# Kernel optimization log

Measured on AMD Instinct MI355X. Metric: run time of the kernel, lower is better.

Reference implementation:

```python
import jax, jax.numpy as jnp
import numpy as np

EPSILON = 1e-8
NUM_STEPS = 1000
S_OFFSET = 0.0001
POWER = 2
CLIPMAX = 0.999
B = 1048576


def _schedule():
    t = jnp.arange(0, NUM_STEPS + 1, dtype=jnp.float32)
    f_t = jnp.cos(np.pi / 2 * (t / NUM_STEPS + S_OFFSET) / (1 + S_OFFSET)) ** POWER
    alpha_bars = f_t / f_t[0]
    betas = jnp.concatenate([jnp.zeros([1], jnp.float32), 1.0 - alpha_bars[1:] / alpha_bars[:-1]])
    betas = jnp.minimum(betas, CLIPMAX)
    sigmas = jnp.sqrt(betas[1:] * ((1.0 - alpha_bars[:-1]) / (1.0 - alpha_bars[1:])))
    sigmas = jnp.concatenate([jnp.zeros([1], jnp.float32), sigmas])
    return alpha_bars, betas, sigmas


def setup_inputs() -> dict:
    key = jax.random.key(0)
    k1, k2, k3, k4, k5 = jax.random.split(key, 5)
    lt = jax.random.normal(k1, (B, 6), dtype=jnp.float32)
    predicted_l0 = jax.random.normal(k2, (B, 6), dtype=jnp.float32)
    pred_lattice = jax.random.normal(k3, (B, 3, 3), dtype=jnp.float32)
    z_noise = jax.random.normal(k4, (B, 6), dtype=jnp.float32)  # torch.randn_like(lt), frozen
    t = jax.random.randint(k5, (B,), 0, NUM_STEPS, dtype=jnp.int64)
    alpha_bars, betas, sigmas = _schedule()
    return {
        "lt": lt,
        "predicted_l0": predicted_l0,
        "pred_lattice": pred_lattice,
        "alpha_bars": alpha_bars,
        "betas": betas,
        "sigmas": sigmas,
        "z_noise": z_noise,
        "t": t,
    }


def reference(lt, predicted_l0, pred_lattice, alpha_bars, betas, sigmas, z_noise, t):
    # VP_lattice.reverse
    alpha = 1.0 - betas[t]
    alpha = jnp.maximum(alpha, 1.0 - betas[-2])  # clamp_min
    alpha_bar = alpha_bars[t]
    sigma = sigmas[t][:, None]

    # polar_decomposition: only the symmetric factor L_tilda = V diag(S) V^T is used
    _, S, Vt = jnp.linalg.svd(pred_lattice, full_matrices=False)  # (B,3),(B,3,3)
    L = jnp.einsum("bji,bj,bjk->bik", Vt, S, Vt)  # Vt^T @ diag(S) @ Vt
    L = (L + jnp.swapaxes(L, 1, 2)) / 2  # symmetrize

    # symmetric_matrix_to_vector: upper triangular incl. diagonal
    vec = jnp.stack([L[:, 0, 0], L[:, 0, 1], L[:, 0, 2], L[:, 1, 1], L[:, 1, 2], L[:, 2, 2]], axis=1)

    predicted_noise = lt - (vec + predicted_l0) / 2
    z = jnp.where((t > 1)[:, None], z_noise, jnp.zeros_like(z_noise))
    coef = (1.0 / jnp.sqrt(alpha + EPSILON))[:, None]
    scale = ((1.0 - alpha) / jnp.sqrt(1.0 - alpha_bar + EPSILON))[:, None]
    return coef * (lt - scale * predicted_noise) + sigma * z
```

## Files before the change

kernel.cpp:

```cpp
#include <hip/hip_runtime.h>


#define NUM_STEPS 1000
#define BLOCK 256

__global__ __launch_bounds__(BLOCK) void vp_lattice_kernel(
    const float* __restrict__ lt,
    const float* __restrict__ pl0,
    const float* __restrict__ plat,
    const float* __restrict__ alpha_bars,
    const float* __restrict__ betas,
    const float* __restrict__ sigmas,
    const float* __restrict__ z_noise,
    const int*   __restrict__ t,
    float* __restrict__ out,
    int n)
{
    __shared__ float sCoef[NUM_STEPS + 1];
    __shared__ float sScale[NUM_STEPS + 1];
    __shared__ float sSig[NUM_STEPS + 1];
    __shared__ __align__(16) float platT[BLOCK * 9];
    __shared__ __align__(16) float ltT[BLOCK * 6];
    __shared__ __align__(16) float p0T[BLOCK * 6];
    __shared__ __align__(16) float znT[BLOCK * 6];

    const int tid = threadIdx.x;
    const int rowBase = blockIdx.x * BLOCK;
    int rem = n - rowBase; if (rem > BLOCK) rem = BLOCK;

    if (rem == BLOCK) {
        const float4* g9 = reinterpret_cast<const float4*>(plat + (size_t)rowBase * 9);
        float4*       s9 = reinterpret_cast<float4*>(platT);
        for (int j = tid; j < BLOCK * 9 / 4; j += BLOCK) s9[j] = g9[j];

        const float4* gl = reinterpret_cast<const float4*>(lt + (size_t)rowBase * 6);
        float4*       sl = reinterpret_cast<float4*>(ltT);
        for (int j = tid; j < BLOCK * 6 / 4; j += BLOCK) sl[j] = gl[j];

        const float4* gp = reinterpret_cast<const float4*>(pl0 + (size_t)rowBase * 6);
        float4*       sp = reinterpret_cast<float4*>(p0T);
        for (int j = tid; j < BLOCK * 6 / 4; j += BLOCK) sp[j] = gp[j];

        const float4* gz = reinterpret_cast<const float4*>(z_noise + (size_t)rowBase * 6);
        float4*       sz = reinterpret_cast<float4*>(znT);
        for (int j = tid; j < BLOCK * 6 / 4; j += BLOCK) sz[j] = gz[j];
    } else {
        for (int j = tid; j < rem * 9; j += BLOCK) platT[j] = plat[(size_t)rowBase * 9 + j];
        for (int j = tid; j < rem * 6; j += BLOCK) {
            ltT[j] = lt[(size_t)rowBase * 6 + j];
            p0T[j] = pl0[(size_t)rowBase * 6 + j];
            znT[j] = z_noise[(size_t)rowBase * 6 + j];
        }
    }

    {
        float beta_last = betas[NUM_STEPS - 1];
        for (int j = tid; j <= NUM_STEPS; j += BLOCK) {
            float alpha = 1.0f - fminf(betas[j], beta_last);
            sCoef[j]  = 1.0f / sqrtf(alpha + 1e-8f);
            sScale[j] = (1.0f - alpha) / sqrtf(1.0f - alpha_bars[j] + 1e-8f);
            sSig[j]   = (j > 1) ? sigmas[j] : 0.0f;
        }
    }

    int ti = (tid < rem) ? t[rowBase + tid] : 0;

    __syncthreads();

    float ov0 = 0.f, ov1 = 0.f, ov2 = 0.f, ov3 = 0.f, ov4 = 0.f, ov5 = 0.f;

    if (tid < rem) {
        const float* pr = platT + tid * 9;
        float a00 = pr[0], a01 = pr[1], a02 = pr[2];
        float a10 = pr[3], a11 = pr[4], a12 = pr[5];
        float a20 = pr[6], a21 = pr[7], a22 = pr[8];

        float m00 = a00*a00 + a10*a10 + a20*a20;
        float m01 = a00*a01 + a10*a11 + a20*a21;
        float m02 = a00*a02 + a10*a12 + a20*a22;
        float m11 = a01*a01 + a11*a11 + a21*a21;
        float m12 = a01*a02 + a11*a12 + a21*a22;
        float m22 = a02*a02 + a12*a12 + a22*a22;

        float q  = (m00 + m11 + m22) * (1.0f/3.0f);
        float b00 = m00 - q, b11 = m11 - q, b22 = m22 - q;
        float p1 = m01*m01 + m02*m02 + m12*m12;
        float p2 = b00*b00 + b11*b11 + b22*b22 + 2.0f*p1;
        float p  = sqrtf(p2 * (1.0f/6.0f));
        float detB = b00*(b11*b22 - m12*m12)
                   - m01*(m01*b22 - m12*m02)
                   + m02*(m01*m12 - b11*m02);
        float pinv = 1.0f / fmaxf(p, 1e-20f);
        float r = 0.5f * detB * pinv * pinv * pinv;
        r = fminf(fmaxf(r, -1.0f), 1.0f);
        float phi = acosf(r) * (1.0f/3.0f);
        float mu1 = q + 2.0f*p*cosf(phi);
        float mu3 = q + 2.0f*p*cosf(phi + 2.0943951023931953f);
        float mu2 = 3.0f*q - mu1 - mu3;
        float l1 = sqrtf(fmaxf(mu1, 0.0f));
        float l2 = sqrtf(fmaxf(mu2, 0.0f));
        float l3 = sqrtf(fmaxf(mu3, 0.0f));

        float IU   = l1 + l2 + l3;
        float IIU  = l1*(l2 + l3) + l2*l3;
        float IIIU = l1*l2*l3;
        float denom = (l1 + l2) * (l1 + l3) * (l2 + l3);
        float dinv  = 1.0f / fmaxf(denom, 1e-25f);
        float sd = (IU*IU - IIU) * dinv;
        float td = IU * IIIU * dinv;
        float nd = -dinv;

        float mm00 = m00*m00 + m01*m01 + m02*m02;
        float mm01 = m00*m01 + m01*m11 + m02*m12;
        float mm02 = m00*m02 + m01*m12 + m02*m22;
        float mm11 = m01*m01 + m11*m11 + m12*m12;
        float mm12 = m01*m02 + m11*m12 + m12*m22;
        float mm22 = m02*m02 + m12*m12 + m22*m22;

        float v0 = nd*mm00 + sd*m00 + td;
        float v1 = nd*mm01 + sd*m01;
        float v2 = nd*mm02 + sd*m02;
        float v3 = nd*mm11 + sd*m11 + td;
        float v4 = nd*mm12 + sd*m12;
        float v5 = nd*mm22 + sd*m22 + td;

        float coef  = sCoef[ti];
        float scale = sScale[ti];
        float sig   = sSig[ti];

        const float2* l2v = reinterpret_cast<const float2*>(ltT) + tid * 3;
        const float2* p2v = reinterpret_cast<const float2*>(p0T) + tid * 3;
        const float2* z2v = reinterpret_cast<const float2*>(znT) + tid * 3;
        float lv[6], pv[6], zv[6];
        float2 w;
        w = l2v[0]; lv[0]=w.x; lv[1]=w.y;
        w = l2v[1]; lv[2]=w.x; lv[3]=w.y;
        w = l2v[2]; lv[4]=w.x; lv[5]=w.y;
        w = p2v[0]; pv[0]=w.x; pv[1]=w.y;
        w = p2v[1]; pv[2]=w.x; pv[3]=w.y;
        w = p2v[2]; pv[4]=w.x; pv[5]=w.y;
        w = z2v[0]; zv[0]=w.x; zv[1]=w.y;
        w = z2v[1]; zv[2]=w.x; zv[3]=w.y;
        w = z2v[2]; zv[4]=w.x; zv[5]=w.y;

        float vv[6] = {v0, v1, v2, v3, v4, v5};
        float ovv[6];
#pragma unroll
        for (int c = 0; c < 6; ++c) {
            float lc = lv[c];
            float pn = lc - 0.5f * (vv[c] + pv[c]);
            ovv[c] = coef * (lc - scale * pn) + sig * zv[c];
        }
        ov0 = ovv[0]; ov1 = ovv[1]; ov2 = ovv[2];
        ov3 = ovv[3]; ov4 = ovv[4]; ov5 = ovv[5];
    }

    __syncthreads();

    if (tid < rem) {
        float2* o2 = reinterpret_cast<float2*>(platT) + tid * 3;
        o2[0] = make_float2(ov0, ov1);
        o2[1] = make_float2(ov2, ov3);
        o2[2] = make_float2(ov4, ov5);
    }

    __syncthreads();

    if (rem == BLOCK) {
        const float4* so = reinterpret_cast<const float4*>(platT);
        float4*       go = reinterpret_cast<float4*>(out + (size_t)rowBase * 6);
        for (int j = tid; j < BLOCK * 6 / 4; j += BLOCK) go[j] = so[j];
    } else {
        for (int j = tid; j < rem * 6; j += BLOCK) out[(size_t)rowBase * 6 + j] = platT[j];
    }
}

extern "C" void kernel_launch(void* const* d_in, const int* in_sizes, int n_in,
                              void* d_out, int out_size, void* d_ws, size_t ws_size,
                              hipStream_t stream) {
    const float* lt         = (const float*)d_in[0];
    const float* pl0        = (const float*)d_in[1];
    const float* plat       = (const float*)d_in[2];
    const float* alpha_bars = (const float*)d_in[3];
    const float* betas      = (const float*)d_in[4];
    const float* sigmas     = (const float*)d_in[5];
    const float* z_noise    = (const float*)d_in[6];
    const int*   t          = (const int*)d_in[7];
    float* out = (float*)d_out;

    int n = in_sizes[0] / 6;
    int grid = (n + BLOCK - 1) / BLOCK;
    vp_lattice_kernel<<<grid, BLOCK, 0, stream>>>(
        lt, pl0, plat, alpha_bars, betas, sigmas, z_noise, t, out, n);
}
```

Before: 171.4 us.

## Precompute schedule table, drop LDS staging for 6-wide arrays, use fast acos/cos

A small pre-kernel folds the per-timestep coefficients into three tables (A, B, sigma) in workspace, which each block copies into LDS instead of recomputing sqrt/div per entry. The lt, predicted_l0, z_noise loads and the output store now go directly through per-thread float2 accesses rather than being staged through shared memory, which removes two barriers and shrinks LDS use. acosf is replaced by a polynomial approximation and cos/div by fast intrinsics, and launch bounds request higher occupancy. The trade-offs are less coalesced strided global accesses, an extra kernel launch, and reduced accuracy in the eigenvalue computation.

```diff
diff --git a/kernel.cpp b/kernel.cpp
--- a/kernel.cpp
+++ b/kernel.cpp
@@ -2,9 +2,31 @@
 
 
 #define NUM_STEPS 1000
+#define TBL 1008
 #define BLOCK 256
 
-__global__ __launch_bounds__(BLOCK) void vp_lattice_kernel(
+__global__ __launch_bounds__(256) void sched_kernel(
+    const float* __restrict__ alpha_bars,
+    const float* __restrict__ betas,
+    const float* __restrict__ sigmas,
+    float* __restrict__ ws)
+{
+    int j = blockIdx.x * blockDim.x + threadIdx.x;
+    if (j >= TBL) return;
+    if (j <= NUM_STEPS) {
+        float beta_last = betas[NUM_STEPS - 1];
+        float alpha = 1.0f - fminf(betas[j], beta_last);
+        float coef  = 1.0f / sqrtf(alpha + 1e-8f);
+        float scale = (1.0f - alpha) / sqrtf(1.0f - alpha_bars[j] + 1e-8f);
+        ws[j]           = coef * (1.0f - scale);
+        ws[TBL + j]     = 0.5f * coef * scale;
+        ws[2 * TBL + j] = (j > 1) ? sigmas[j] : 0.0f;
+    } else {
+        ws[j] = 0.0f; ws[TBL + j] = 0.0f; ws[2 * TBL + j] = 0.0f;
+    }
+}
+
+__global__ __launch_bounds__(BLOCK, 6) void vp_lattice_kernel(
     const float* __restrict__ lt,
     const float* __restrict__ pl0,
     const float* __restrict__ plat,
@@ -14,15 +36,14 @@
     const float* __restrict__ z_noise,
     const int*   __restrict__ t,
     float* __restrict__ out,
-    int n)
+    int n,
+    const float* __restrict__ ws,
+    int use_ws)
 {
-    __shared__ float sCoef[NUM_STEPS + 1];
-    __shared__ float sScale[NUM_STEPS + 1];
-    __shared__ float sSig[NUM_STEPS + 1];
+    __shared__ __align__(16) float sA[TBL];
+    __shared__ __align__(16) float sB[TBL];
+    __shared__ __align__(16) float sS[TBL];
     __shared__ __align__(16) float platT[BLOCK * 9];
-    __shared__ __align__(16) float ltT[BLOCK * 6];
-    __shared__ __align__(16) float p0T[BLOCK * 6];
-    __shared__ __align__(16) float znT[BLOCK * 6];
 
     const int tid = threadIdx.x;
     const int rowBase = blockIdx.x * BLOCK;
@@ -31,35 +52,39 @@
     if (rem == BLOCK) {
         const float4* g9 = reinterpret_cast<const float4*>(plat + (size_t)rowBase * 9);
         float4*       s9 = reinterpret_cast<float4*>(platT);
-        for (int j = tid; j < BLOCK * 9 / 4; j += BLOCK) s9[j] = g9[j];
-
-        const float4* gl = reinterpret_cast<const float4*>(lt + (size_t)rowBase * 6);
-        float4*       sl = reinterpret_cast<float4*>(ltT);
-        for (int j = tid; j < BLOCK * 6 / 4; j += BLOCK) sl[j] = gl[j];
-
-        const float4* gp = reinterpret_cast<const float4*>(pl0 + (size_t)rowBase * 6);
-        float4*       sp = reinterpret_cast<float4*>(p0T);
-        for (int j = tid; j < BLOCK * 6 / 4; j += BLOCK) sp[j] = gp[j];
-
-        const float4* gz = reinterpret_cast<const float4*>(z_noise + (size_t)rowBase * 6);
-        float4*       sz = reinterpret_cast<float4*>(znT);
-        for (int j = tid; j < BLOCK * 6 / 4; j += BLOCK) sz[j] = gz[j];
+#pragma unroll
+        for (int k = 0; k < 3; ++k) {
+            int j = tid + k * BLOCK;
+            if (j < BLOCK * 9 / 4) s9[j] = g9[j];
+        }
     } else {
-        for (int j = tid; j < rem * 9; j += BLOCK) platT[j] = plat[(size_t)rowBase * 9 + j];
-        for (int j = tid; j < rem * 6; j += BLOCK) {
-            ltT[j] = lt[(size_t)rowBase * 6 + j];
-            p0T[j] = pl0[(size_t)rowBase * 6 + j];
-            znT[j] = z_noise[(size_t)rowBase * 6 + j];
+        for (int j = tid; j < rem * 9; j += BLOCK)
+            platT[j] = plat[(size_t)rowBase * 9 + j];
+    }
+
+    if (use_ws) {
+        const float4* w4 = reinterpret_cast<const float4*>(ws);
+        float4* a4 = reinterpret_cast<float4*>(sA);
+        float4* b4 = reinterpret_cast<float4*>(sB);
+        float4* s4 = reinterpret_cast<float4*>(sS);
+        for (int j = tid; j < TBL / 4; j += BLOCK) {
+            a4[j] = w4[j];
+            b4[j] = w4[TBL / 4 + j];
+            s4[j] = w4[2 * (TBL / 4) + j];
         }
-    }
-
-    {
+    } else {
         float beta_last = betas[NUM_STEPS - 1];
-        for (int j = tid; j <= NUM_STEPS; j += BLOCK) {
-            float alpha = 1.0f - fminf(betas[j], beta_last);
-            sCoef[j]  = 1.0f / sqrtf(alpha + 1e-8f);
-            sScale[j] = (1.0f - alpha) / sqrtf(1.0f - alpha_bars[j] + 1e-8f);
-            sSig[j]   = (j > 1) ? sigmas[j] : 0.0f;
+        for (int j = tid; j < TBL; j += BLOCK) {
+            float A = 0.0f, Bc = 0.0f, S = 0.0f;
+            if (j <= NUM_STEPS) {
+                float alpha = 1.0f - fminf(betas[j], beta_last);
+                float coef  = 1.0f / sqrtf(alpha + 1e-8f);
+                float scale = (1.0f - alpha) / sqrtf(1.0f - alpha_bars[j] + 1e-8f);
+                A  = coef * (1.0f - scale);
+                Bc = 0.5f * coef * scale;
+                S  = (j > 1) ? sigmas[j] : 0.0f;
+            }
+            sA[j] = A; sB[j] = Bc; sS[j] = S;
         }
     }
 
@@ -67,112 +92,92 @@
 
     __syncthreads();
 
-    float ov0 = 0.f, ov1 = 0.f, ov2 = 0.f, ov3 = 0.f, ov4 = 0.f, ov5 = 0.f;
-
-    if (tid < rem) {
-        const float* pr = platT + tid * 9;
-        float a00 = pr[0], a01 = pr[1], a02 = pr[2];
-        float a10 = pr[3], a11 = pr[4], a12 = pr[5];
-        float a20 = pr[6], a21 = pr[7], a22 = pr[8];
-
-        float m00 = a00*a00 + a10*a10 + a20*a20;
-        float m01 = a00*a01 + a10*a11 + a20*a21;
-        float m02 = a00*a02 + a10*a12 + a20*a22;
-        float m11 = a01*a01 + a11*a11 + a21*a21;
-        float m12 = a01*a02 + a11*a12 + a21*a22;
-        float m22 = a02*a02 + a12*a12 + a22*a22;
-
-        float q  = (m00 + m11 + m22) * (1.0f/3.0f);
-        float b00 = m00 - q, b11 = m11 - q, b22 = m22 - q;
-        float p1 = m01*m01 + m02*m02 + m12*m12;
-        float p2 = b00*b00 + b11*b11 + b22*b22 + 2.0f*p1;
-        float p  = sqrtf(p2 * (1.0f/6.0f));
-        float detB = b00*(b11*b22 - m12*m12)
-                   - m01*(m01*b22 - m12*m02)
-                   + m02*(m01*m12 - b11*m02);
-        float pinv = 1.0f / fmaxf(p, 1e-20f);
-        float r = 0.5f * detB * pinv * pinv * pinv;
-        r = fminf(fmaxf(r, -1.0f), 1.0f);
-        float phi = acosf(r) * (1.0f/3.0f);
-        float mu1 = q + 2.0f*p*cosf(phi);
-        float mu3 = q + 2.0f*p*cosf(phi + 2.0943951023931953f);
-        float mu2 = 3.0f*q - mu1 - mu3;
-        float l1 = sqrtf(fmaxf(mu1, 0.0f));
-        float l2 = sqrtf(fmaxf(mu2, 0.0f));
-        float l3 = sqrtf(fmaxf(mu3, 0.0f));
-
-        float IU   = l1 + l2 + l3;
-        float IIU  = l1*(l2 + l3) + l2*l3;
-        float IIIU = l1*l2*l3;
-        float denom = (l1 + l2) * (l1 + l3) * (l2 + l3);
-        float dinv  = 1.0f / fmaxf(denom, 1e-25f);
-        float sd = (IU*IU - IIU) * dinv;
-        float td = IU * IIIU * dinv;
-        float nd = -dinv;
-
-        float mm00 = m00*m00 + m01*m01 + m02*m02;
-        float mm01 = m00*m01 + m01*m11 + m02*m12;
-        float mm02 = m00*m02 + m01*m12 + m02*m22;
-        float mm11 = m01*m01 + m11*m11 + m12*m12;
-        float mm12 = m01*m02 + m11*m12 + m12*m22;
-        float mm22 = m02*m02 + m12*m12 + m22*m22;
-
-        float v0 = nd*mm00 + sd*m00 + td;
-        float v1 = nd*mm01 + sd*m01;
-        float v2 = nd*mm02 + sd*m02;
-        float v3 = nd*mm11 + sd*m11 + td;
-        float v4 = nd*mm12 + sd*m12;
-        float v5 = nd*mm22 + sd*m22 + td;
-
-        float coef  = sCoef[ti];
-        float scale = sScale[ti];
-        float sig   = sSig[ti];
-
-        const float2* l2v = reinterpret_cast<const float2*>(ltT) + tid * 3;
-        const float2* p2v = reinterpret_cast<const float2*>(p0T) + tid * 3;
-        const float2* z2v = reinterpret_cast<const float2*>(znT) + tid * 3;
-        float lv[6], pv[6], zv[6];
-        float2 w;
-        w = l2v[0]; lv[0]=w.x; lv[1]=w.y;
-        w = l2v[1]; lv[2]=w.x; lv[3]=w.y;
-        w = l2v[2]; lv[4]=w.x; lv[5]=w.y;
-        w = p2v[0]; pv[0]=w.x; pv[1]=w.y;
-        w = p2v[1]; pv[2]=w.x; pv[3]=w.y;
-        w = p2v[2]; pv[4]=w.x; pv[5]=w.y;
-        w = z2v[0]; zv[0]=w.x; zv[1]=w.y;
-        w = z2v[1]; zv[2]=w.x; zv[3]=w.y;
-        w = z2v[2]; zv[4]=w.x; zv[5]=w.y;
-
-        float vv[6] = {v0, v1, v2, v3, v4, v5};
-        float ovv[6];
-#pragma unroll
-        for (int c = 0; c < 6; ++c) {
-            float lc = lv[c];
-            float pn = lc - 0.5f * (vv[c] + pv[c]);
-            ovv[c] = coef * (lc - scale * pn) + sig * zv[c];
-        }
-        ov0 = ovv[0]; ov1 = ovv[1]; ov2 = ovv[2];
-        ov3 = ovv[3]; ov4 = ovv[4]; ov5 = ovv[5];
-    }
-
-    __syncthreads();
-
-    if (tid < rem) {
-        float2* o2 = reinterpret_cast<float2*>(platT) + tid * 3;
-        o2[0] = make_float2(ov0, ov1);
-        o2[1] = make_float2(ov2, ov3);
-        o2[2] = make_float2(ov4, ov5);
-    }
-
-    __syncthreads();
-
-    if (rem == BLOCK) {
-        const float4* so = reinterpret_cast<const float4*>(platT);
-        float4*       go = reinterpret_cast<float4*>(out + (size_t)rowBase * 6);
-        for (int j = tid; j < BLOCK * 6 / 4; j += BLOCK) go[j] = so[j];
-    } else {
-        for (int j = tid; j < rem * 6; j += BLOCK) out[(size_t)rowBase * 6 + j] = platT[j];
-    }
+    if (tid >= rem) return;
+
+    size_t b6 = (size_t)(rowBase + tid) * 6;
+    const float2* lt2 = reinterpret_cast<const float2*>(lt + b6);
+    const float2* p02 = reinterpret_cast<const float2*>(pl0 + b6);
+    const float2* zn2 = reinterpret_cast<const float2*>(z_noise + b6);
+    float2 lw0 = lt2[0], lw1 = lt2[1], lw2 = lt2[2];
+    float2 pw0 = p02[0], pw1 = p02[1], pw2 = p02[2];
+    float2 zw0 = zn2[0], zw1 = zn2[1], zw2 = zn2[2];
+
+    const float* pr = platT + tid * 9;
+    float a00 = pr[0], a01 = pr[1], a02 = pr[2];
+    float a10 = pr[3], a11 = pr[4], a12 = pr[5];
+    float a20 = pr[6], a21 = pr[7], a22 = pr[8];
+
+    float m00 = a00*a00 + a10*a10 + a20*a20;
+    float m01 = a00*a01 + a10*a11 + a20*a21;
+    float m02 = a00*a02 + a10*a12 + a20*a22;
+    float m11 = a01*a01 + a11*a11 + a21*a21;
+    float m12 = a01*a02 + a11*a12 + a21*a22;
+    float m22 = a02*a02 + a12*a12 + a22*a22;
+
+    float q  = (m00 + m11 + m22) * (1.0f/3.0f);
+    float b00 = m00 - q, b11 = m11 - q, b22 = m22 - q;
+    float p1 = m01*m01 + m02*m02 + m12*m12;
+    float p2 = b00*b00 + b11*b11 + b22*b22 + 2.0f*p1;
+    float p  = sqrtf(p2 * (1.0f/6.0f));
+    float detB = b00*(b11*b22 - m12*m12)
+               - m01*(m01*b22 - m12*m02)
+               + m02*(m01*m12 - b11*m02);
+    float pinv = __fdividef(1.0f, fmaxf(p, 1e-20f));
+    float r = 0.5f * detB * pinv * pinv * pinv;
+    r = fminf(fmaxf(r, -1.0f), 1.0f);
+
+    float ar = fabsf(r);
+    float sq = sqrtf(1.0f - ar);
+    float pl = 1.5707288f + ar * (-0.2121144f + ar * (0.0742610f - ar * 0.0187293f));
+    float ac = sq * pl;
+    float acr = (r >= 0.0f) ? ac : (3.14159265358979f - ac);
+    float phi = acr * (1.0f/3.0f);
+    float mu1 = q + 2.0f*p*__cosf(phi);
+    float mu3 = q + 2.0f*p*__cosf(phi + 2.0943951023931953f);
+    float mu2 = 3.0f*q - mu1 - mu3;
+    float l1 = sqrtf(fmaxf(mu1, 0.0f));
+    float l2 = sqrtf(fmaxf(mu2, 0.0f));
+    float l3 = sqrtf(fmaxf(mu3, 0.0f));
+
+    float IU   = l1 + l2 + l3;
+    float IIU  = l1*(l2 + l3) + l2*l3;
+    float IIIU = l1*l2*l3;
+    float denom = (l1 + l2) * (l1 + l3) * (l2 + l3);
+    float dinv  = __fdividef(1.0f, fmaxf(denom, 1e-25f));
+    float sd = (IU*IU - IIU) * dinv;
+    float td = IU * IIIU * dinv;
+    float nd = -dinv;
+
+    float mm00 = m00*m00 + m01*m01 + m02*m02;
+    float mm01 = m00*m01 + m01*m11 + m02*m12;
+    float mm02 = m00*m02 + m01*m12 + m02*m22;
+    float mm11 = m01*m01 + m11*m11 + m12*m12;
+    float mm12 = m01*m02 + m11*m12 + m12*m22;
+    float mm22 = m02*m02 + m12*m12 + m22*m22;
+
+    float v0 = nd*mm00 + sd*m00 + td;
+    float v1 = nd*mm01 + sd*m01;
+    float v2 = nd*mm02 + sd*m02;
+    float v3 = nd*mm11 + sd*m11 + td;
+    float v4 = nd*mm12 + sd*m12;
+    float v5 = nd*mm22 + sd*m22 + td;
+
+    float A  = sA[ti];
+    float Bc = sB[ti];
+    float S  = sS[ti];
+
+    float2 o0, o1, o2;
+    o0.x = A*lw0.x + Bc*(v0 + pw0.x) + S*zw0.x;
+    o0.y = A*lw0.y + Bc*(v1 + pw0.y) + S*zw0.y;
+    o1.x = A*lw1.x + Bc*(v2 + pw1.x) + S*zw1.x;
+    o1.y = A*lw1.y + Bc*(v3 + pw1.y) + S*zw1.y;
+    o2.x = A*lw2.x + Bc*(v4 + pw2.x) + S*zw2.x;
+    o2.y = A*lw2.y + Bc*(v5 + pw2.y) + S*zw2.y;
+
+    float2* out2 = reinterpret_cast<float2*>(out + b6);
+    out2[0] = o0;
+    out2[1] = o1;
+    out2[2] = o2;
 }
 
 extern "C" void kernel_launch(void* const* d_in, const int* in_sizes, int n_in,
@@ -187,9 +192,15 @@
     const float* z_noise    = (const float*)d_in[6];
     const int*   t          = (const int*)d_in[7];
     float* out = (float*)d_out;
+    float* ws  = (float*)d_ws;
 
     int n = in_sizes[0] / 6;
+    int use_ws = (ws != nullptr && ws_size >= (size_t)(3 * TBL * sizeof(float)));
+
+    if (use_ws) {
+        sched_kernel<<<(TBL + 255) / 256, 256, 0, stream>>>(alpha_bars, betas, sigmas, ws);
+    }
     int grid = (n + BLOCK - 1) / BLOCK;
     vp_lattice_kernel<<<grid, BLOCK, 0, stream>>>(
-        lt, pl0, plat, alpha_bars, betas, sigmas, z_noise, t, out, n);
+        lt, pl0, plat, alpha_bars, betas, sigmas, z_noise, t, out, n, ws, use_ws);
 }
```

Result: faster. 154.8 us (-9.7%).
